# Optimization experiments

Measured on AMD Instinct MI355X. Metric: run time of the kernel, lower is better.

The kernel has to match this reference:

```python
import jax, jax.numpy as jnp
import numpy as np

R = 5   # num edge types
T = 3   # num node types
N = 50000
IN, HID, OUT = 256, 256, 128


def setup_inputs() -> dict:
    key = jax.random.key(0)
    ks = jax.random.split(key, 20)
    n0, n1, n2 = 16667, 16667, 16666
    x0 = jax.random.normal(ks[0], (n0, IN), jnp.float32)
    x1 = jax.random.normal(ks[1], (n1, IN), jnp.float32)
    emb2 = jax.random.normal(ks[2], (n2, IN), jnp.float32)  # learned embedding (xavier-like)
    E = 1600000
    edge_index = jax.random.randint(ks[3], (2, E), 0, N, dtype=jnp.int64)
    edge_type = jax.random.randint(ks[4], (E,), 0, R, dtype=jnp.int64)
    node_type = jax.random.randint(ks[5], (N,), 0, T, dtype=jnp.int64)
    local_node_idx = jax.random.randint(ks[6], (N,), 0, n2, dtype=jnp.int64)  # valid for all types

    def lin_w(k, o, i):
        return jax.random.normal(k, (o, i), jnp.float32) / np.sqrt(i).astype(np.float32)

    dims = [(IN, HID), (HID, HID), (HID, OUT)]
    params = {}
    ki = 7
    for l, (di, do) in enumerate(dims):
        params[f"rel_W{l}"] = jnp.stack([lin_w(jax.random.fold_in(ks[ki], r), do, di) for r in range(R)])
        params[f"root_W{l}"] = jnp.stack([lin_w(jax.random.fold_in(ks[ki + 1], t), do, di) for t in range(T)])
        params[f"root_b{l}"] = jnp.zeros((T, do), jnp.float32)
        ki += 2
    return dict(x0=x0, x1=x1, emb2=emb2,
                edge_index=edge_index, edge_type=edge_type,
                node_type=node_type, local_node_idx=local_node_idx, **params)


def _group_input(x_list, node_type, local_node_idx):
    # scatter per-type features into flat [N, IN]
    h = jnp.zeros((node_type.shape[0], x_list[0].shape[1]), x_list[0].dtype)
    for t, xt in enumerate(x_list):
        mask = (node_type == t)[:, None].astype(xt.dtype)
        h = h + mask * xt[local_node_idx]  # local_node_idx is always in-range
    return h


def _conv(x, rel_W, root_W, root_b, src, dst, edge_type, node_type):
    n = x.shape[0]
    # per-(target node, relation) mean aggregation in one segmented reduction
    seg = dst * R + edge_type
    msgs = x[src]                                              # [E, Din]
    sums = jax.ops.segment_sum(msgs, seg, num_segments=n * R)  # [N*R, Din]
    cnt = jax.ops.segment_sum(jnp.ones((seg.shape[0],), x.dtype), seg, num_segments=n * R)
    mean = (sums / jnp.maximum(cnt, 1.0)[:, None]).reshape(n, R, -1)
    out = jnp.einsum('nrd,rod->no', mean, rel_W)
    # per-node-type root transform (with bias)
    for t in range(T):
        mask = (node_type == t)[:, None].astype(x.dtype)
        out = out + mask * (x @ root_W[t].T + root_b[t])
    return out


def reference(x0, x1, emb2,
              rel_W0, root_W0, root_b0,
              rel_W1, root_W1, root_b1,
              rel_W2, root_W2, root_b2,
              edge_index, edge_type, node_type, local_node_idx):
    src, dst = edge_index[0], edge_index[1]
    x = _group_input([x0, x1, emb2], node_type, local_node_idx)
    layers = [(rel_W0, root_W0, root_b0), (rel_W1, root_W1, root_b1), (rel_W2, root_W2, root_b2)]
    for i, (rw, gw, gb) in enumerate(layers):
        x = _conv(x, rw, gw, gb, src, dst, edge_type, node_type)
        if i != len(layers) - 1:
            x = jax.nn.relu(x)  # eval mode: dropout is identity
    return jax.nn.log_softmax(x, axis=-1)
```

## Files before the change

### kernel.cpp

```cpp
#include <hip/hip_runtime.h>
#include <hip/hip_bf16.h>
#include <hip/hip_fp8.h>
#include <stdint.h>

#define N_NODES 50000
#define M_PAD   50048
#define N_EDGES 1600000
#define R_REL   5
#define NBUCK   391
#define NB1     256
#define EPB     6250
#define BH_N    (NBUCK * NB1)
#define GS_BLOCKS 98
#define STAGE_CAP 6144
#define HIST_BLOCKS 196

typedef __bf16 bf16;
typedef __bf16 bf16x2 __attribute__((ext_vector_type(2)));
typedef __bf16 bf16x4 __attribute__((ext_vector_type(4)));
typedef __bf16 bf16x8 __attribute__((ext_vector_type(8)));
typedef float  f32x2  __attribute__((ext_vector_type(2)));
typedef float  f32x4  __attribute__((ext_vector_type(4)));

#define GLOAD_LDS16(g, l)                                                          \
    __builtin_amdgcn_global_load_lds(                                              \
        (const __attribute__((address_space(1))) void*)(g),                        \
        (__attribute__((address_space(3))) void*)(l), 16, 0, 0)

__device__ __forceinline__ uint8_t f32_to_fp8(float f) {
    return __hip_fp8_e4m3(f).__x;
}
__device__ __forceinline__ float fp8_to_f32(uint32_t b) {
    __hip_fp8_e4m3 v; v.__x = (uint8_t)b; return (float)v;
}

__device__ __forceinline__ void fp8_accum4(uint32_t bits, float ww, float* s) {
#if __has_builtin(__builtin_amdgcn_cvt_pk_f32_fp8)
    f32x2 lo = __builtin_amdgcn_cvt_pk_f32_fp8((int)bits, false);
    f32x2 hi = __builtin_amdgcn_cvt_pk_f32_fp8((int)bits, true);
    s[0] += ww * lo[0]; s[1] += ww * lo[1];
    s[2] += ww * hi[0]; s[3] += ww * hi[1];
#else
    s[0] += ww * fp8_to_f32(bits & 0xFF);
    s[1] += ww * fp8_to_f32((bits >> 8) & 0xFF);
    s[2] += ww * fp8_to_f32((bits >> 16) & 0xFF);
    s[3] += ww * fp8_to_f32(bits >> 24);
#endif
}

__global__ __launch_bounds__(256) void group_input_k(
    const float* __restrict__ x0, const float* __restrict__ x1,
    const float* __restrict__ emb2, const int* __restrict__ ntype,
    const int* __restrict__ lidx, bf16* __restrict__ h)
{
    int row = blockIdx.x * 4 + (threadIdx.x >> 6);
    int lane = threadIdx.x & 63;
    if (row >= N_NODES) return;
    int t = ntype[row];
    int li = lidx[row];
    const float* src = (t == 0) ? x0 : (t == 1) ? x1 : emb2;
    float4 v = *reinterpret_cast<const float4*>(&src[(size_t)li * 256 + lane * 4]);
    bf16x4 o;
    o[0] = (bf16)v.x; o[1] = (bf16)v.y; o[2] = (bf16)v.z; o[3] = (bf16)v.w;
    *reinterpret_cast<bf16x4*>(&h[(size_t)row * 256 + lane * 4]) = o;
}

__global__ __launch_bounds__(256) void bucket_hist_k(
    const int* __restrict__ ei, int* __restrict__ bh)
{
    __shared__ int lds[NBUCK];
    int t = threadIdx.x;
    for (int i = t; i < NBUCK; i += 256) lds[i] = 0;
    __syncthreads();
    int base = blockIdx.x * EPB;
    for (int i = t; i < EPB; i += 256) {
        int dst = ei[N_EDGES + base + i];
        atomicAdd(&lds[dst >> 7], 1);
    }
    __syncthreads();
    for (int i = t; i < NBUCK; i += 256) bh[i * NB1 + blockIdx.x] = lds[i];
}

__global__ __launch_bounds__(256) void gscan1_k(
    const int* __restrict__ in, int* __restrict__ outv,
    int* __restrict__ blksum, int n)
{
    __shared__ int lds[256];
    int base = blockIdx.x * 1024;
    int t = threadIdx.x;
    int vals[4]; int s = 0;
#pragma unroll
    for (int i = 0; i < 4; ++i) {
        int idx = base + t * 4 + i;
        vals[i] = (idx < n) ? in[idx] : 0;
        s += vals[i];
    }
    lds[t] = s;
    __syncthreads();
    for (int off = 1; off < 256; off <<= 1) {
        int v = (t >= off) ? lds[t - off] : 0;
        __syncthreads();
        lds[t] += v;
        __syncthreads();
    }
    int incl = lds[t];
    int ex = incl - s;
    if (t == 255) blksum[blockIdx.x] = incl;
    int run = ex;
#pragma unroll
    for (int i = 0; i < 4; ++i) {
        int idx = base + t * 4 + i;
        if (idx < n) outv[idx] = run;
        run += vals[i];
    }
}

__global__ __launch_bounds__(256) void gscan2_k(int* __restrict__ blksum, int nblk)
{
    __shared__ int lds[256];
    int t = threadIdx.x;
    int v = (t < nblk) ? blksum[t] : 0;
    lds[t] = v;
    __syncthreads();
    for (int off = 1; off < 256; off <<= 1) {
        int u = (t >= off) ? lds[t - off] : 0;
        __syncthreads();
        lds[t] += u;
        __syncthreads();
    }
    if (t < nblk) blksum[t] = lds[t] - v;
}

__global__ __launch_bounds__(256) void gfold_k(
    int* __restrict__ outv, const int* __restrict__ blksum, int n)
{
    int base = blockIdx.x * 1024 + threadIdx.x * 4;
    int b = blksum[blockIdx.x];
#pragma unroll
    for (int i = 0; i < 4; ++i) {
        int idx = base + i;
        if (idx < n) outv[idx] += b;
    }
}

__global__ __launch_bounds__(256) void bucket_scatter_k(
    const int* __restrict__ ei, const int* __restrict__ et,
    const int* __restrict__ bhs, uint32_t* __restrict__ ebuf)
{
    __shared__ int cur[NBUCK];
    int t = threadIdx.x;
    for (int i = t; i < NBUCK; i += 256) cur[i] = bhs[i * NB1 + blockIdx.x];
    __syncthreads();
    int base = blockIdx.x * EPB;
    for (int i = t; i < EPB; i += 256) {
        int e = base + i;
        int src = ei[e];
        int dst = ei[N_EDGES + e];
        int r = et[e];
        int pos = atomicAdd(&cur[dst >> 7], 1);
        ebuf[pos] = (uint32_t)(src * R_REL + r) | ((uint32_t)(dst & 127) << 25);
    }
}

__global__ __launch_bounds__(256) void bucket_rank_k(
    const uint32_t* __restrict__ ebuf, const int* __restrict__ bhs,
    uint32_t* __restrict__ pk, int* __restrict__ noff)
{
    __shared__ uint32_t se[STAGE_CAP];
    __shared__ int hist[640];
    __shared__ int cursor[640];
    __shared__ int sb[256];
    int t = threadIdx.x;
    int b = blockIdx.x;
    int start = bhs[b * NB1];
    int end = (b < NBUCK - 1) ? bhs[(b + 1) * NB1] : N_EDGES;
    int size = end - start;
    for (int i = t; i < 640; i += 256) hist[i] = 0;
    __syncthreads();
    for (int i = t; i < size; i += 256) {
        uint32_t v = ebuf[start + i];
        if (i < STAGE_CAP) se[i] = v;
        uint32_t sr = v & 0x3FFFFu;
        int r = (int)(sr % 5u);
        int seg = (int)(v >> 25) * R_REL + r;
        atomicAdd(&hist[seg], 1);
    }
    __syncthreads();
    int b0 = t * 3;
    int loc[3]; int s0 = 0;
#pragma unroll
    for (int j = 0; j < 3; ++j) {
        int idx = b0 + j;
        int v = (idx < 640) ? hist[idx] : 0;
        loc[j] = s0; s0 += v;
    }
    sb[t] = s0;
    __syncthreads();
    for (int off = 1; off < 256; off <<= 1) {
        int u = (t >= off) ? sb[t - off] : 0;
        __syncthreads();
        sb[t] += u;
        __syncthreads();
    }
    int pre = sb[t] - s0;
#pragma unroll
    for (int j = 0; j < 3; ++j) {
        int idx = b0 + j;
        if (idx < 640) cursor[idx] = start + pre + loc[j];
    }
    __syncthreads();
    if (t < 128) noff[b * 128 + t] = cursor[t * 5];
    if (b == NBUCK - 1 && t == 128) noff[M_PAD] = N_EDGES;
    __syncthreads();
    for (int i = t; i < size; i += 256) {
        uint32_t v = (i < STAGE_CAP) ? se[i] : ebuf[start + i];
        uint32_t sr = v & 0x3FFFFu;
        int r = (int)(sr % 5u);
        int seg = (int)(v >> 25) * R_REL + r;
        int pos = atomicAdd(&cursor[seg], 1);
        pk[pos] = sr | ((uint32_t)hist[seg] << 18);
    }
}

__global__ __launch_bounds__(256) void typed_hist_k(
    const int* __restrict__ ntype, int* __restrict__ tcnt)
{
    __shared__ int c[3];
    if (threadIdx.x < 3) c[threadIdx.x] = 0;
    __syncthreads();
    int n = blockIdx.x * 256 + threadIdx.x;
    if (n < N_NODES) atomicAdd(&c[ntype[n]], 1);
    __syncthreads();
    if (threadIdx.x < 3) tcnt[threadIdx.x * HIST_BLOCKS + blockIdx.x] = c[threadIdx.x];
}

__global__ __launch_bounds__(1024) void typed_scan_k(
    const int* __restrict__ tcnt, int* __restrict__ toff, int* __restrict__ meta)
{
    __shared__ int lds[1024];
    int t = threadIdx.x;
    int v = (t < 3 * HIST_BLOCKS) ? tcnt[t] : 0;
    lds[t] = v;
    __syncthreads();
    for (int off = 1; off < 1024; off <<= 1) {
        int u = (t >= off) ? lds[t - off] : 0;
        __syncthreads();
        lds[t] += u;
        __syncthreads();
    }
    if (t < 3 * HIST_BLOCKS) toff[t] = lds[t] - v;
    if (t == 0) {
        int ts1 = lds[1 * HIST_BLOCKS - 1];
        int ts2 = lds[2 * HIST_BLOCKS - 1];
        int ts3 = lds[3 * HIST_BLOCKS - 1];
        meta[0] = 0; meta[1] = ts1; meta[2] = ts2; meta[3] = ts3;
        int c0 = ts1, c1 = ts2 - ts1, c2 = ts3 - ts2;
        meta[8] = c0; meta[9] = c1; meta[10] = c2;
        int b0 = (c0 + 127) >> 7, b1 = (c1 + 127) >> 7, b2 = (c2 + 127) >> 7;
        meta[4] = 0; meta[5] = b0; meta[6] = b0 + b1; meta[7] = b0 + b1 + b2;
    }
}

__global__ __launch_bounds__(256) void typed_scatter_k(
    const int* __restrict__ ntype, const int* __restrict__ toff,
    int* __restrict__ perm)
{
    __shared__ int cur[3];
    if (threadIdx.x < 3) cur[threadIdx.x] = 0;
    __syncthreads();
    int n = blockIdx.x * 256 + threadIdx.x;
    if (n < N_NODES) {
        int t = ntype[n];
        int rank = atomicAdd(&cur[t], 1);
        perm[toff[t * HIST_BLOCKS + blockIdx.x] + rank] = n;
    }
}

__global__ __launch_bounds__(256) void cast_w_k(
    const float* __restrict__ relW, const float* __restrict__ rootW,
    bf16* __restrict__ Wt, bf16* __restrict__ Rt, int relN, int rootN)
{
    int i = blockIdx.x * 256 + threadIdx.x;
    if (i < relN)  Wt[i] = (bf16)relW[i];
    if (i < rootN) Rt[i] = (bf16)rootW[i];
}

__global__ __launch_bounds__(256) void gemm_y_f8_k(
    const bf16* __restrict__ A, const bf16* __restrict__ B,
    uint8_t* __restrict__ Y, int ldc, int NT)
{
    __shared__ bf16 As[128][64];
    __shared__ bf16 Bs[128][64];
    int bid = blockIdx.x;
    int xcd = bid & 7;
    int r2 = bid >> 3;
    int ml = r2 / NT, nt = r2 - ml * NT;
    int m = xcd * 49 + ml;
    if (m >= M_PAD / 128) return;
    int m0 = m * 128, n0 = nt * 128;
    int tid = threadIdx.x;
    int lane = tid & 63, wave = tid >> 6;
    int wm = wave >> 1, wn = wave & 1;

    f32x4 acc[4][4] = {};

    for (int kt = 0; kt < 4; ++kt) {
#pragma unroll
        for (int cc = 0; cc < 4; ++cc) {
            int linear = cc * 256 + tid;
            int row = linear >> 3, sl = linear & 7;
            const bf16* gA = &A[(size_t)(m0 + row) * 256 + kt * 64 + sl * 8];
            const bf16* gB = &B[(size_t)(n0 + row) * 256 + kt * 64 + sl * 8];
            char* sA = (char*)&As[0][0] + (size_t)(cc * 256 + wave * 64) * 16;
            char* sB = (char*)&Bs[0][0] + (size_t)(cc * 256 + wave * 64) * 16;
            GLOAD_LDS16(gA, sA);
            GLOAD_LDS16(gB, sB);
        }
        __syncthreads();
#pragma unroll
        for (int kk = 0; kk < 2; ++kk) {
            bf16x8 af[4], bfr[4];
            int k0 = kk * 32 + (lane >> 4) * 8;
#pragma unroll
            for (int i = 0; i < 4; ++i) {
                af[i]  = *reinterpret_cast<const bf16x8*>(&As[wm * 64 + i * 16 + (lane & 15)][k0]);
                bfr[i] = *reinterpret_cast<const bf16x8*>(&Bs[wn * 64 + i * 16 + (lane & 15)][k0]);
            }
#pragma unroll
            for (int i = 0; i < 4; ++i)
#pragma unroll
                for (int j = 0; j < 4; ++j)
                    acc[i][j] = __builtin_amdgcn_mfma_f32_16x16x32_bf16(af[i], bfr[j], acc[i][j], 0, 0, 0);
        }
        __syncthreads();
    }

#pragma unroll
    for (int i = 0; i < 4; ++i)
#pragma unroll
        for (int j = 0; j < 4; ++j)
#pragma unroll
            for (int r = 0; r < 4; ++r) {
                int row = m0 + wm * 64 + i * 16 + (lane >> 4) * 4 + r;
                int col = n0 + wn * 64 + j * 16 + (lane & 15);
                Y[(size_t)row * ldc + col] = f32_to_fp8(acc[i][j][r]);
            }
}

__global__ __launch_bounds__(256) void gemm_y_bf_k(
    const bf16* __restrict__ A, const bf16* __restrict__ B,
    bf16* __restrict__ Y, int ldc, int NT)
{
    __shared__ bf16 As[128][64];
    __shared__ bf16 Bs[128][64];
    int bid = blockIdx.x;
    int xcd = bid & 7;
    int r2 = bid >> 3;
    int ml = r2 / NT, nt = r2 - ml * NT;
    int m = xcd * 49 + ml;
    if (m >= M_PAD / 128) return;
    int m0 = m * 128, n0 = nt * 128;
    int tid = threadIdx.x;
    int lane = tid & 63, wave = tid >> 6;
    int wm = wave >> 1, wn = wave & 1;

    f32x4 acc[4][4] = {};

    for (int kt = 0; kt < 4; ++kt) {
#pragma unroll
        for (int cc = 0; cc < 4; ++cc) {
            int linear = cc * 256 + tid;
            int row = linear >> 3, sl = linear & 7;
            const bf16* gA = &A[(size_t)(m0 + row) * 256 + kt * 64 + sl * 8];
            const bf16* gB = &B[(size_t)(n0 + row) * 256 + kt * 64 + sl * 8];
            char* sA = (char*)&As[0][0] + (size_t)(cc * 256 + wave * 64) * 16;
            char* sB = (char*)&Bs[0][0] + (size_t)(cc * 256 + wave * 64) * 16;
            GLOAD_LDS16(gA, sA);
            GLOAD_LDS16(gB, sB);
        }
        __syncthreads();
#pragma unroll
        for (int kk = 0; kk < 2; ++kk) {
            bf16x8 af[4], bfr[4];
            int k0 = kk * 32 + (lane >> 4) * 8;
#pragma unroll
            for (int i = 0; i < 4; ++i) {
                af[i]  = *reinterpret_cast<const bf16x8*>(&As[wm * 64 + i * 16 + (lane & 15)][k0]);
                bfr[i] = *reinterpret_cast<const bf16x8*>(&Bs[wn * 64 + i * 16 + (lane & 15)][k0]);
            }
#pragma unroll
            for (int i = 0; i < 4; ++i)
#pragma unroll
                for (int j = 0; j < 4; ++j)
                    acc[i][j] = __builtin_amdgcn_mfma_f32_16x16x32_bf16(af[i], bfr[j], acc[i][j], 0, 0, 0);
        }
        __syncthreads();
    }

#pragma unroll
    for (int i = 0; i < 4; ++i)
#pragma unroll
        for (int j = 0; j < 4; ++j)
#pragma unroll
            for (int r = 0; r < 4; ++r) {
                int row = m0 + wm * 64 + i * 16 + (lane >> 4) * 4 + r;
                int col = n0 + wn * 64 + j * 16 + (lane & 15);
                Y[(size_t)row * ldc + col] = (bf16)acc[i][j][r];
            }
}

__global__ __launch_bounds__(256) void gather_f8_k(
    const uint8_t* __restrict__ Y, const uint32_t* __restrict__ pk,
    const int* __restrict__ noff, bf16* __restrict__ Cb)
{
    int wave = threadIdx.x >> 6, lane = threadIdx.x & 63;
    int n = blockIdx.x * 4 + wave;
    if (n >= N_NODES) return;
    int off0 = noff[n];
    int c = noff[n + 1] - off0;

    float s[4] = {};
    int e = 0;
    for (; e + 16 <= c; e += 16) {
        uint32_t w[16]; uint32_t v[16];
#pragma unroll
        for (int j = 0; j < 16; ++j) w[j] = pk[off0 + e + j];
#pragma unroll
        for (int j = 0; j < 16; ++j)
            v[j] = *reinterpret_cast<const uint32_t*>(&Y[(size_t)(w[j] & 0x3FFFF) * 256 + lane * 4]);
#pragma unroll
        for (int j = 0; j < 16; ++j) {
            float ww = __builtin_amdgcn_rcpf((float)(w[j] >> 18));
            fp8_accum4(v[j], ww, s);
        }
    }
    if (e + 8 <= c) {
        uint32_t w[8]; uint32_t v[8];
#pragma unroll
        for (int j = 0; j < 8; ++j) w[j] = pk[off0 + e + j];
#pragma unroll
        for (int j = 0; j < 8; ++j)
            v[j] = *reinterpret_cast<const uint32_t*>(&Y[(size_t)(w[j] & 0x3FFFF) * 256 + lane * 4]);
#pragma unroll
        for (int j = 0; j < 8; ++j) {
            float ww = __builtin_amdgcn_rcpf((float)(w[j] >> 18));
            fp8_accum4(v[j], ww, s);
        }
        e += 8;
    }
    if (e + 4 <= c) {
        uint32_t w[4]; uint32_t v[4];
#pragma unroll
        for (int j = 0; j < 4; ++j) w[j] = pk[off0 + e + j];
#pragma unroll
        for (int j = 0; j < 4; ++j)
            v[j] = *reinterpret_cast<const uint32_t*>(&Y[(size_t)(w[j] & 0x3FFFF) * 256 + lane * 4]);
#pragma unroll
        for (int j = 0; j < 4; ++j) {
            float ww = __builtin_amdgcn_rcpf((float)(w[j] >> 18));
            fp8_accum4(v[j], ww, s);
        }
        e += 4;
    }
    for (; e < c; ++e) {
        uint32_t w = pk[off0 + e];
        uint32_t v = *reinterpret_cast<const uint32_t*>(&Y[(size_t)(w & 0x3FFFF) * 256 + lane * 4]);
        float ww = __builtin_amdgcn_rcpf((float)(w >> 18));
        fp8_accum4(v, ww, s);
    }

    bf16x4 o;
#pragma unroll
    for (int q = 0; q < 4; ++q) o[q] = (bf16)s[q];
    *reinterpret_cast<bf16x4*>(&Cb[(size_t)n * 256 + lane * 4]) = o;
}

__global__ __launch_bounds__(256) void gather_bf_k(
    const bf16* __restrict__ Y, const uint32_t* __restrict__ pk,
    const int* __restrict__ noff, bf16* __restrict__ Cb)
{
    int wave = threadIdx.x >> 6, lane = threadIdx.x & 63;
    int n = blockIdx.x * 4 + wave;
    if (n >= N_NODES) return;
    int off0 = noff[n];
    int c = noff[n + 1] - off0;

    float s0 = 0.f, s1 = 0.f;
    int e = 0;
    for (; e + 16 <= c; e += 16) {
        uint32_t w[16]; bf16x2 v[16];
#pragma unroll
        for (int j = 0; j < 16; ++j) w[j] = pk[off0 + e + j];
#pragma unroll
        for (int j = 0; j < 16; ++j)
            v[j] = *reinterpret_cast<const bf16x2*>(&Y[(size_t)(w[j] & 0x3FFFF) * 128 + lane * 2]);
#pragma unroll
        for (int j = 0; j < 16; ++j) {
            float ww = __builtin_amdgcn_rcpf((float)(w[j] >> 18));
            s0 += ww * (float)v[j][0];
            s1 += ww * (float)v[j][1];
        }
    }
    if (e + 8 <= c) {
        uint32_t w[8]; bf16x2 v[8];
#pragma unroll
        for (int j = 0; j < 8; ++j) w[j] = pk[off0 + e + j];
#pragma unroll
        for (int j = 0; j < 8; ++j)
            v[j] = *reinterpret_cast<const bf16x2*>(&Y[(size_t)(w[j] & 0x3FFFF) * 128 + lane * 2]);
#pragma unroll
        for (int j = 0; j < 8; ++j) {
            float ww = __builtin_amdgcn_rcpf((float)(w[j] >> 18));
            s0 += ww * (float)v[j][0];
            s1 += ww * (float)v[j][1];
        }
        e += 8;
    }
    if (e + 4 <= c) {
        uint32_t w[4]; bf16x2 v[4];
#pragma unroll
        for (int j = 0; j < 4; ++j) w[j] = pk[off0 + e + j];
#pragma unroll
        for (int j = 0; j < 4; ++j)
            v[j] = *reinterpret_cast<const bf16x2*>(&Y[(size_t)(w[j] & 0x3FFFF) * 128 + lane * 2]);
#pragma unroll
        for (int j = 0; j < 4; ++j) {
            float ww = __builtin_amdgcn_rcpf((float)(w[j] >> 18));
            s0 += ww * (float)v[j][0];
            s1 += ww * (float)v[j][1];
        }
        e += 4;
    }
    for (; e < c; ++e) {
        uint32_t w = pk[off0 + e];
        bf16x2 v = *reinterpret_cast<const bf16x2*>(&Y[(size_t)(w & 0x3FFFF) * 128 + lane * 2]);
        float ww = __builtin_amdgcn_rcpf((float)(w >> 18));
        s0 += ww * (float)v[0];
        s1 += ww * (float)v[1];
    }

    bf16x2 o; o[0] = (bf16)s0; o[1] = (bf16)s1;
    *reinterpret_cast<bf16x2*>(&Cb[(size_t)n * 128 + lane * 2]) = o;
}

__global__ __launch_bounds__(256) void gemm_root_k(
    const bf16* __restrict__ h, const bf16* __restrict__ Rt,
    const float* __restrict__ rootB, const int* __restrict__ perm,
    const int* __restrict__ meta, const bf16* __restrict__ Cb,
    float* __restrict__ C, bf16* __restrict__ hout, int Dout, int relu_mode)
{
    __shared__ bf16 As[128][64];
    __shared__ bf16 Bs[128][64];
    __shared__ int ridx[128];
    int tid = threadIdx.x;
    int bx = blockIdx.x;
    int b1 = meta[5], b2 = meta[6], b3 = meta[7];
    if (bx >= b3) return;
    int t = (bx >= b2) ? 2 : (bx >= b1 ? 1 : 0);
    int chunk = bx - (t == 2 ? b2 : (t == 1 ? b1 : 0));
    int tstart = meta[t];
    int tc = meta[8 + t];
    int rbase = chunk * 128;
    if (tid < 128) {
        int lr = rbase + tid;
        ridx[tid] = (lr < tc) ? perm[tstart + lr] : 0;
    }
    __syncthreads();

    int lane = tid & 63, wave = tid >> 6;
    int wm = wave >> 1, wn = wave & 1;
    int n0 = blockIdx.y * 128;
    const bf16* B = Rt + (size_t)t * Dout * 256;

    f32x4 acc[4][4] = {};

    for (int kt = 0; kt < 4; ++kt) {
#pragma unroll
        for (int cc = 0; cc < 4; ++cc) {
            int linear = cc * 256 + tid;
            int row = linear >> 3, sl = linear & 7;
            const bf16* gA = &h[(size_t)ridx[row] * 256 + kt * 64 + sl * 8];
            const bf16* gB = &B[(size_t)(n0 + row) * 256 + kt * 64 + sl * 8];
            char* sA = (char*)&As[0][0] + (size_t)(cc * 256 + wave * 64) * 16;
            char* sB = (char*)&Bs[0][0] + (size_t)(cc * 256 + wave * 64) * 16;
            GLOAD_LDS16(gA, sA);
            GLOAD_LDS16(gB, sB);
        }
        __syncthreads();
#pragma unroll
        for (int kk = 0; kk < 2; ++kk) {
            bf16x8 af[4], bfr[4];
            int k0 = kk * 32 + (lane >> 4) * 8;
#pragma unroll
            for (int i = 0; i < 4; ++i) {
                af[i]  = *reinterpret_cast<const bf16x8*>(&As[wm * 64 + i * 16 + (lane & 15)][k0]);
                bfr[i] = *reinterpret_cast<const bf16x8*>(&Bs[wn * 64 + i * 16 + (lane & 15)][k0]);
            }
#pragma unroll
            for (int i = 0; i < 4; ++i)
#pragma unroll
                for (int j = 0; j < 4; ++j)
                    acc[i][j] = __builtin_amdgcn_mfma_f32_16x16x32_bf16(af[i], bfr[j], acc[i][j], 0, 0, 0);
        }
        __syncthreads();
    }

#pragma unroll
    for (int i = 0; i < 4; ++i)
#pragma unroll
        for (int j = 0; j < 4; ++j)
#pragma unroll
            for (int r = 0; r < 4; ++r) {
                int rl = wm * 64 + i * 16 + (lane >> 4) * 4 + r;
                int col = n0 + wn * 64 + j * 16 + (lane & 15);
                if (rbase + rl < tc) {
                    int ri = ridx[rl];
                    float v = (float)Cb[(size_t)ri * Dout + col] + acc[i][j][r]
                              + rootB[t * Dout + col];
                    if (relu_mode)
                        hout[(size_t)ri * Dout + col] = (bf16)fmaxf(v, 0.f);
                    else
                        C[(size_t)ri * Dout + col] = v;
                }
            }
}

__global__ __launch_bounds__(256) void logsoftmax_k(
    const float* __restrict__ C, float* __restrict__ out, int M)
{
    int row = blockIdx.x * 4 + (threadIdx.x >> 6);
    int lane = threadIdx.x & 63;
    if (row >= M) return;
    float v0 = C[(size_t)row * 128 + lane];
    float v1 = C[(size_t)row * 128 + 64 + lane];
    float m = fmaxf(v0, v1);
    for (int off = 32; off; off >>= 1) m = fmaxf(m, __shfl_xor(m, off));
    float s = expf(v0 - m) + expf(v1 - m);
    for (int off = 32; off; off >>= 1) s += __shfl_xor(s, off);
    float lse = m + logf(s);
    out[(size_t)row * 128 + lane] = v0 - lse;
    out[(size_t)row * 128 + 64 + lane] = v1 - lse;
}

extern "C" void kernel_launch(void* const* d_in, const int* in_sizes, int n_in,
                              void* d_out, int out_size, void* d_ws, size_t ws_size,
                              hipStream_t stream)
{
    const float* x0   = (const float*)d_in[0];
    const float* x1   = (const float*)d_in[1];
    const float* emb2 = (const float*)d_in[2];
    const int*   ei   = (const int*)d_in[3];
    const int*   et   = (const int*)d_in[4];
    const int*   ntyp = (const int*)d_in[5];
    const int*   lidx = (const int*)d_in[6];
    const float* relW[3]  = {(const float*)d_in[7],  (const float*)d_in[10], (const float*)d_in[13]};
    const float* rootW[3] = {(const float*)d_in[8],  (const float*)d_in[11], (const float*)d_in[14]};
    const float* rootB[3] = {(const float*)d_in[9],  (const float*)d_in[12], (const float*)d_in[15]};
    float* out = (float*)d_out;

    char* p = (char*)d_ws;
    auto carve = [&](size_t bytes) {
        char* q = p;
        p += (bytes + 255) & ~(size_t)255;
        return (void*)q;
    };
    bf16* h_a   = (bf16*)carve((size_t)M_PAD * 256 * 2);
    bf16* h_b   = (bf16*)carve((size_t)M_PAD * 256 * 2);
    uint8_t* Yq = (uint8_t*)carve((size_t)M_PAD * 1280);
    bf16* Yb    = (bf16*)Yq;
    bf16* Cb    = (bf16*)carve((size_t)M_PAD * 256 * 2);
    float* C    = (float*)carve((size_t)M_PAD * 128 * 4);
    bf16* WtA   = (bf16*)carve((size_t)(2 * R_REL * 256 * 256 + R_REL * 128 * 256) * 2);
    bf16* RtA   = (bf16*)carve((size_t)(2 * 3 * 256 * 256 + 3 * 128 * 256) * 2);
    int* bh     = (int*)carve((size_t)BH_N * 4);
    int* bhs    = (int*)carve((size_t)BH_N * 4);
    int* gblk   = (int*)carve((size_t)256 * 4);
    uint32_t* ebuf = (uint32_t*)carve((size_t)N_EDGES * 4);
    uint32_t* pk   = (uint32_t*)carve((size_t)N_EDGES * 4);
    int* noff   = (int*)carve((size_t)(M_PAD + 1) * 4);
    int* tcnt   = (int*)carve((size_t)3 * HIST_BLOCKS * 4);
    int* toff   = (int*)carve((size_t)3 * HIST_BLOCKS * 4);
    int* meta   = (int*)carve((size_t)16 * 4);
    int* perm   = (int*)carve((size_t)N_NODES * 4);

    bf16* Wt[3] = {WtA, WtA + (size_t)R_REL * 256 * 256, WtA + (size_t)2 * R_REL * 256 * 256};
    bf16* Rt[3] = {RtA, RtA + (size_t)3 * 256 * 256, RtA + (size_t)2 * 3 * 256 * 256};

    group_input_k<<<(N_NODES + 3) / 4, 256, 0, stream>>>(x0, x1, emb2, ntyp, lidx, h_a);
    bucket_hist_k<<<NB1, 256, 0, stream>>>(ei, bh);
    gscan1_k<<<GS_BLOCKS, 256, 0, stream>>>(bh, bhs, gblk, BH_N);
    gscan2_k<<<1, 256, 0, stream>>>(gblk, GS_BLOCKS);
    gfold_k<<<GS_BLOCKS, 256, 0, stream>>>(bhs, gblk, BH_N);
    bucket_scatter_k<<<NB1, 256, 0, stream>>>(ei, et, bhs, ebuf);
    bucket_rank_k<<<NBUCK, 256, 0, stream>>>(ebuf, bhs, pk, noff);
    typed_hist_k<<<HIST_BLOCKS, 256, 0, stream>>>(ntyp, tcnt);
    typed_scan_k<<<1, 1024, 0, stream>>>(tcnt, toff, meta);
    typed_scatter_k<<<HIST_BLOCKS, 256, 0, stream>>>(ntyp, toff, perm);
    const int douts[3] = {256, 256, 128};
    for (int l = 0; l < 3; ++l)
        cast_w_k<<<(R_REL * douts[l] * 256 + 255) / 256, 256, 0, stream>>>(
            relW[l], rootW[l], Wt[l], Rt[l], R_REL * douts[l] * 256, 3 * douts[l] * 256);

    bf16* cur = h_a;
    bf16* nxt = h_b;
    for (int l = 0; l < 3; ++l) {
        if (l < 2) {
            gemm_y_f8_k<<<49 * 10 * 8, 256, 0, stream>>>(cur, Wt[l], Yq, 1280, 10);
            gather_f8_k<<<(N_NODES + 3) / 4, 256, 0, stream>>>(Yq, pk, noff, Cb);
            gemm_root_k<<<dim3(393, 2), 256, 0, stream>>>(
                cur, Rt[l], rootB[l], perm, meta, Cb, C, nxt, 256, 1);
        } else {
            gemm_y_bf_k<<<49 * 5 * 8, 256, 0, stream>>>(cur, Wt[l], Yb, 640, 5);
            gather_bf_k<<<(N_NODES + 3) / 4, 256, 0, stream>>>(Yb, pk, noff, Cb);
            gemm_root_k<<<dim3(393, 1), 256, 0, stream>>>(
                cur, Rt[l], rootB[l], perm, meta, Cb, C, nxt, 128, 0);
        }
        bf16* tmp = cur; cur = nxt; nxt = tmp;
    }
    logsoftmax_k<<<(N_NODES + 3) / 4, 256, 0, stream>>>(C, out, N_NODES);
}
```

Baseline: 525.5 us.

## Merge setup kernels, fuse log-softmax into final root GEMM, pack fp8 conversions

Merges the independent preprocessing kernels (input grouping, bucket histogram, type histogram, weight casts) into one block-indexed launch. It also combines the two small scans and the fold/typed scatter steps, cutting the number of kernel launches. Log-softmax is fused into the last root GEMM through an LDS tile, so the fp32 intermediate no longer makes a round trip to global memory. FP8 output quantization now uses packed conversion instructions. The costs are higher LDS use in the final GEMM (64KB for the L tile), which lowers occupancy, and an in-place scan on bh.

```diff
diff --git a/kernel.cpp b/kernel.cpp
--- a/kernel.cpp
+++ b/kernel.cpp
@@ -14,6 +14,7 @@
 #define GS_BLOCKS 98
 #define STAGE_CAP 6144
 #define HIST_BLOCKS 196
+#define GI_BLOCKS 12500
 
 typedef __bf16 bf16;
 typedef __bf16 bf16x2 __attribute__((ext_vector_type(2)));
@@ -32,6 +33,17 @@
 }
 __device__ __forceinline__ float fp8_to_f32(uint32_t b) {
     __hip_fp8_e4m3 v; v.__x = (uint8_t)b; return (float)v;
+}
+
+__device__ __forceinline__ uint32_t fp8_pack4(float a0, float a1, float a2, float a3) {
+#if __has_builtin(__builtin_amdgcn_cvt_pk_fp8_f32)
+    int q = __builtin_amdgcn_cvt_pk_fp8_f32(a0, a1, 0, false);
+    q = __builtin_amdgcn_cvt_pk_fp8_f32(a2, a3, q, true);
+    return (uint32_t)q;
+#else
+    return (uint32_t)f32_to_fp8(a0) | ((uint32_t)f32_to_fp8(a1) << 8) |
+           ((uint32_t)f32_to_fp8(a2) << 16) | ((uint32_t)f32_to_fp8(a3) << 24);
+#endif
 }
 
 __device__ __forceinline__ void fp8_accum4(uint32_t bits, float ww, float* s) {
@@ -48,37 +60,67 @@
 #endif
 }
 
-__global__ __launch_bounds__(256) void group_input_k(
+__global__ __launch_bounds__(256) void setup1_k(
     const float* __restrict__ x0, const float* __restrict__ x1,
     const float* __restrict__ emb2, const int* __restrict__ ntype,
-    const int* __restrict__ lidx, bf16* __restrict__ h)
-{
-    int row = blockIdx.x * 4 + (threadIdx.x >> 6);
-    int lane = threadIdx.x & 63;
-    if (row >= N_NODES) return;
-    int t = ntype[row];
-    int li = lidx[row];
-    const float* src = (t == 0) ? x0 : (t == 1) ? x1 : emb2;
-    float4 v = *reinterpret_cast<const float4*>(&src[(size_t)li * 256 + lane * 4]);
-    bf16x4 o;
-    o[0] = (bf16)v.x; o[1] = (bf16)v.y; o[2] = (bf16)v.z; o[3] = (bf16)v.w;
-    *reinterpret_cast<bf16x4*>(&h[(size_t)row * 256 + lane * 4]) = o;
-}
-
-__global__ __launch_bounds__(256) void bucket_hist_k(
-    const int* __restrict__ ei, int* __restrict__ bh)
-{
-    __shared__ int lds[NBUCK];
+    const int* __restrict__ lidx, bf16* __restrict__ h,
+    const int* __restrict__ ei, int* __restrict__ bh,
+    int* __restrict__ tcnt,
+    const float* __restrict__ relW0, const float* __restrict__ rootW0,
+    const float* __restrict__ relW1, const float* __restrict__ rootW1,
+    const float* __restrict__ relW2, const float* __restrict__ rootW2,
+    bf16* __restrict__ Wt0, bf16* __restrict__ Rt0,
+    bf16* __restrict__ Wt1, bf16* __restrict__ Rt1,
+    bf16* __restrict__ Wt2, bf16* __restrict__ Rt2)
+{
+    __shared__ int smem[NBUCK];
+    int bid = blockIdx.x;
     int t = threadIdx.x;
-    for (int i = t; i < NBUCK; i += 256) lds[i] = 0;
-    __syncthreads();
-    int base = blockIdx.x * EPB;
-    for (int i = t; i < EPB; i += 256) {
-        int dst = ei[N_EDGES + base + i];
-        atomicAdd(&lds[dst >> 7], 1);
-    }
-    __syncthreads();
-    for (int i = t; i < NBUCK; i += 256) bh[i * NB1 + blockIdx.x] = lds[i];
+    if (bid < GI_BLOCKS) {
+        int row = bid * 4 + (t >> 6);
+        int lane = t & 63;
+        int ty = ntype[row];
+        int li = lidx[row];
+        const float* src = (ty == 0) ? x0 : (ty == 1) ? x1 : emb2;
+        float4 v = *reinterpret_cast<const float4*>(&src[(size_t)li * 256 + lane * 4]);
+        bf16x4 o;
+        o[0] = (bf16)v.x; o[1] = (bf16)v.y; o[2] = (bf16)v.z; o[3] = (bf16)v.w;
+        *reinterpret_cast<bf16x4*>(&h[(size_t)row * 256 + lane * 4]) = o;
+        return;
+    }
+    bid -= GI_BLOCKS;
+    if (bid < NB1) {
+        for (int i = t; i < NBUCK; i += 256) smem[i] = 0;
+        __syncthreads();
+        int base = bid * EPB;
+        for (int i = t; i < EPB; i += 256) {
+            int dst = ei[N_EDGES + base + i];
+            atomicAdd(&smem[dst >> 7], 1);
+        }
+        __syncthreads();
+        for (int i = t; i < NBUCK; i += 256) bh[i * NB1 + bid] = smem[i];
+        return;
+    }
+    bid -= NB1;
+    if (bid < HIST_BLOCKS) {
+        if (t < 3) smem[t] = 0;
+        __syncthreads();
+        int n = bid * 256 + t;
+        if (n < N_NODES) atomicAdd(&smem[ntype[n]], 1);
+        __syncthreads();
+        if (t < 3) tcnt[t * HIST_BLOCKS + bid] = smem[t];
+        return;
+    }
+    bid -= HIST_BLOCKS;
+    const float* relW; const float* rootW; bf16* Wt; bf16* Rt; int Dout;
+    if (bid < 1280)      { relW = relW0; rootW = rootW0; Wt = Wt0; Rt = Rt0; Dout = 256; }
+    else if (bid < 2560) { relW = relW1; rootW = rootW1; Wt = Wt1; Rt = Rt1; Dout = 256; bid -= 1280; }
+    else                 { relW = relW2; rootW = rootW2; Wt = Wt2; Rt = Rt2; Dout = 128; bid -= 2560; }
+    int i = bid * 256 + t;
+    int relN = R_REL * Dout * 256;
+    if (i < relN)  Wt[i] = (bf16)relW[i];
+    int rootN = 3 * Dout * 256;
+    if (i < rootN) Rt[i] = (bf16)rootW[i];
 }
 
 __global__ __launch_bounds__(256) void gscan1_k(
@@ -115,31 +157,73 @@
     }
 }
 
-__global__ __launch_bounds__(256) void gscan2_k(int* __restrict__ blksum, int nblk)
-{
-    __shared__ int lds[256];
+__global__ __launch_bounds__(1024) void scan2m_k(
+    int* __restrict__ gblk,
+    const int* __restrict__ tcnt, int* __restrict__ toff, int* __restrict__ meta)
+{
+    __shared__ int lds[1024];
     int t = threadIdx.x;
-    int v = (t < nblk) ? blksum[t] : 0;
+    if (blockIdx.x == 0) {
+        int v = (t < GS_BLOCKS) ? gblk[t] : 0;
+        lds[t] = v;
+        __syncthreads();
+        for (int off = 1; off < 1024; off <<= 1) {
+            int u = (t >= off) ? lds[t - off] : 0;
+            __syncthreads();
+            lds[t] += u;
+            __syncthreads();
+        }
+        if (t < GS_BLOCKS) gblk[t] = lds[t] - v;
+        return;
+    }
+    int v = (t < 3 * HIST_BLOCKS) ? tcnt[t] : 0;
     lds[t] = v;
     __syncthreads();
-    for (int off = 1; off < 256; off <<= 1) {
+    for (int off = 1; off < 1024; off <<= 1) {
         int u = (t >= off) ? lds[t - off] : 0;
         __syncthreads();
         lds[t] += u;
         __syncthreads();
     }
-    if (t < nblk) blksum[t] = lds[t] - v;
-}
-
-__global__ __launch_bounds__(256) void gfold_k(
-    int* __restrict__ outv, const int* __restrict__ blksum, int n)
-{
-    int base = blockIdx.x * 1024 + threadIdx.x * 4;
-    int b = blksum[blockIdx.x];
-#pragma unroll
-    for (int i = 0; i < 4; ++i) {
-        int idx = base + i;
-        if (idx < n) outv[idx] += b;
+    if (t < 3 * HIST_BLOCKS) toff[t] = lds[t] - v;
+    if (t == 0) {
+        int ts1 = lds[1 * HIST_BLOCKS - 1];
+        int ts2 = lds[2 * HIST_BLOCKS - 1];
+        int ts3 = lds[3 * HIST_BLOCKS - 1];
+        meta[0] = 0; meta[1] = ts1; meta[2] = ts2; meta[3] = ts3;
+        int c0 = ts1, c1 = ts2 - ts1, c2 = ts3 - ts2;
+        meta[8] = c0; meta[9] = c1; meta[10] = c2;
+        int b0 = (c0 + 127) >> 7, b1 = (c1 + 127) >> 7, b2 = (c2 + 127) >> 7;
+        meta[4] = 0; meta[5] = b0; meta[6] = b0 + b1; meta[7] = b0 + b1 + b2;
+    }
+}
+
+__global__ __launch_bounds__(256) void setup3_k(
+    int* __restrict__ bhs, const int* __restrict__ gblk,
+    const int* __restrict__ ntype, const int* __restrict__ toff,
+    int* __restrict__ perm)
+{
+    __shared__ int cur[3];
+    int bid = blockIdx.x;
+    int t = threadIdx.x;
+    if (bid < GS_BLOCKS) {
+        int base = bid * 1024 + t * 4;
+        int b = gblk[bid];
+#pragma unroll
+        for (int i = 0; i < 4; ++i) {
+            int idx = base + i;
+            if (idx < BH_N) bhs[idx] += b;
+        }
+        return;
+    }
+    bid -= GS_BLOCKS;
+    if (t < 3) cur[t] = 0;
+    __syncthreads();
+    int n = bid * 256 + t;
+    if (n < N_NODES) {
+        int ty = ntype[n];
+        int rank = atomicAdd(&cur[ty], 1);
+        perm[toff[ty * HIST_BLOCKS + bid] + rank] = n;
     }
 }
 
@@ -220,69 +304,6 @@
         int pos = atomicAdd(&cursor[seg], 1);
         pk[pos] = sr | ((uint32_t)hist[seg] << 18);
     }
-}
-
-__global__ __launch_bounds__(256) void typed_hist_k(
-    const int* __restrict__ ntype, int* __restrict__ tcnt)
-{
-    __shared__ int c[3];
-    if (threadIdx.x < 3) c[threadIdx.x] = 0;
-    __syncthreads();
-    int n = blockIdx.x * 256 + threadIdx.x;
-    if (n < N_NODES) atomicAdd(&c[ntype[n]], 1);
-    __syncthreads();
-    if (threadIdx.x < 3) tcnt[threadIdx.x * HIST_BLOCKS + blockIdx.x] = c[threadIdx.x];
-}
-
-__global__ __launch_bounds__(1024) void typed_scan_k(
-    const int* __restrict__ tcnt, int* __restrict__ toff, int* __restrict__ meta)
-{
-    __shared__ int lds[1024];
-    int t = threadIdx.x;
-    int v = (t < 3 * HIST_BLOCKS) ? tcnt[t] : 0;
-    lds[t] = v;
-    __syncthreads();
-    for (int off = 1; off < 1024; off <<= 1) {
-        int u = (t >= off) ? lds[t - off] : 0;
-        __syncthreads();
-        lds[t] += u;
-        __syncthreads();
-    }
-    if (t < 3 * HIST_BLOCKS) toff[t] = lds[t] - v;
-    if (t == 0) {
-        int ts1 = lds[1 * HIST_BLOCKS - 1];
-        int ts2 = lds[2 * HIST_BLOCKS - 1];
-        int ts3 = lds[3 * HIST_BLOCKS - 1];
-        meta[0] = 0; meta[1] = ts1; meta[2] = ts2; meta[3] = ts3;
-        int c0 = ts1, c1 = ts2 - ts1, c2 = ts3 - ts2;
-        meta[8] = c0; meta[9] = c1; meta[10] = c2;
-        int b0 = (c0 + 127) >> 7, b1 = (c1 + 127) >> 7, b2 = (c2 + 127) >> 7;
-        meta[4] = 0; meta[5] = b0; meta[6] = b0 + b1; meta[7] = b0 + b1 + b2;
-    }
-}
-
-__global__ __launch_bounds__(256) void typed_scatter_k(
-    const int* __restrict__ ntype, const int* __restrict__ toff,
-    int* __restrict__ perm)
-{
-    __shared__ int cur[3];
-    if (threadIdx.x < 3) cur[threadIdx.x] = 0;
-    __syncthreads();
-    int n = blockIdx.x * 256 + threadIdx.x;
-    if (n < N_NODES) {
-        int t = ntype[n];
-        int rank = atomicAdd(&cur[t], 1);
-        perm[toff[t * HIST_BLOCKS + blockIdx.x] + rank] = n;
-    }
-}
-
-__global__ __launch_bounds__(256) void cast_w_k(
-    const float* __restrict__ relW, const float* __restrict__ rootW,
-    bf16* __restrict__ Wt, bf16* __restrict__ Rt, int relN, int rootN)
-{
-    int i = blockIdx.x * 256 + threadIdx.x;
-    if (i < relN)  Wt[i] = (bf16)relW[i];
-    if (i < rootN) Rt[i] = (bf16)rootW[i];
 }
 
 __global__ __launch_bounds__(256) void gemm_y_f8_k(
@@ -338,13 +359,15 @@
 #pragma unroll
     for (int i = 0; i < 4; ++i)
 #pragma unroll
-        for (int j = 0; j < 4; ++j)
-#pragma unroll
-            for (int r = 0; r < 4; ++r) {
-                int row = m0 + wm * 64 + i * 16 + (lane >> 4) * 4 + r;
-                int col = n0 + wn * 64 + j * 16 + (lane & 15);
-                Y[(size_t)row * ldc + col] = f32_to_fp8(acc[i][j][r]);
-            }
+        for (int j = 0; j < 4; ++j) {
+            uint32_t q = fp8_pack4(acc[i][j][0], acc[i][j][1], acc[i][j][2], acc[i][j][3]);
+            int row0 = m0 + wm * 64 + i * 16 + (lane >> 4) * 4;
+            int col = n0 + wn * 64 + j * 16 + (lane & 15);
+            Y[(size_t)(row0 + 0) * ldc + col] = (uint8_t)q;
+            Y[(size_t)(row0 + 1) * ldc + col] = (uint8_t)(q >> 8);
+            Y[(size_t)(row0 + 2) * ldc + col] = (uint8_t)(q >> 16);
+            Y[(size_t)(row0 + 3) * ldc + col] = (uint8_t)(q >> 24);
+        }
 }
 
 __global__ __launch_bounds__(256) void gemm_y_bf_k(
@@ -547,7 +570,7 @@
     const bf16* __restrict__ h, const bf16* __restrict__ Rt,
     const float* __restrict__ rootB, const int* __restrict__ perm,
     const int* __restrict__ meta, const bf16* __restrict__ Cb,
-    float* __restrict__ C, bf16* __restrict__ hout, int Dout, int relu_mode)
+    bf16* __restrict__ hout, int Dout)
 {
     __shared__ bf16 As[128][64];
     __shared__ bf16 Bs[128][64];
@@ -617,29 +640,102 @@
                     int ri = ridx[rl];
                     float v = (float)Cb[(size_t)ri * Dout + col] + acc[i][j][r]
                               + rootB[t * Dout + col];
-                    if (relu_mode)
-                        hout[(size_t)ri * Dout + col] = (bf16)fmaxf(v, 0.f);
-                    else
-                        C[(size_t)ri * Dout + col] = v;
+                    hout[(size_t)ri * Dout + col] = (bf16)fmaxf(v, 0.f);
                 }
             }
 }
 
-__global__ __launch_bounds__(256) void logsoftmax_k(
-    const float* __restrict__ C, float* __restrict__ out, int M)
-{
-    int row = blockIdx.x * 4 + (threadIdx.x >> 6);
-    int lane = threadIdx.x & 63;
-    if (row >= M) return;
-    float v0 = C[(size_t)row * 128 + lane];
-    float v1 = C[(size_t)row * 128 + 64 + lane];
-    float m = fmaxf(v0, v1);
-    for (int off = 32; off; off >>= 1) m = fmaxf(m, __shfl_xor(m, off));
-    float s = expf(v0 - m) + expf(v1 - m);
-    for (int off = 32; off; off >>= 1) s += __shfl_xor(s, off);
-    float lse = m + logf(s);
-    out[(size_t)row * 128 + lane] = v0 - lse;
-    out[(size_t)row * 128 + 64 + lane] = v1 - lse;
+__global__ __launch_bounds__(256) void gemm_root_ls_k(
+    const bf16* __restrict__ h, const bf16* __restrict__ Rt,
+    const float* __restrict__ rootB, const int* __restrict__ perm,
+    const int* __restrict__ meta, const bf16* __restrict__ Cb,
+    float* __restrict__ out)
+{
+    __shared__ bf16 As[128][64];
+    __shared__ bf16 Bs[128][64];
+    __shared__ int ridx[128];
+    __shared__ float L[128][128];
+    const int Dout = 128;
+    int tid = threadIdx.x;
+    int bx = blockIdx.x;
+    int b1 = meta[5], b2 = meta[6], b3 = meta[7];
+    if (bx >= b3) return;
+    int t = (bx >= b2) ? 2 : (bx >= b1 ? 1 : 0);
+    int chunk = bx - (t == 2 ? b2 : (t == 1 ? b1 : 0));
+    int tstart = meta[t];
+    int tc = meta[8 + t];
+    int rbase = chunk * 128;
+    if (tid < 128) {
+        int lr = rbase + tid;
+        ridx[tid] = (lr < tc) ? perm[tstart + lr] : 0;
+    }
+    __syncthreads();
+
+    int lane = tid & 63, wave = tid >> 6;
+    int wm = wave >> 1, wn = wave & 1;
+    const bf16* B = Rt + (size_t)t * Dout * 256;
+
+    f32x4 acc[4][4] = {};
+
+    for (int kt = 0; kt < 4; ++kt) {
+#pragma unroll
+        for (int cc = 0; cc < 4; ++cc) {
+            int linear = cc * 256 + tid;
+            int row = linear >> 3, sl = linear & 7;
+            const bf16* gA = &h[(size_t)ridx[row] * 256 + kt * 64 + sl * 8];
+            const bf16* gB = &B[(size_t)(row) * 256 + kt * 64 + sl * 8];
+            char* sA = (char*)&As[0][0] + (size_t)(cc * 256 + wave * 64) * 16;
+            char* sB = (char*)&Bs[0][0] + (size_t)(cc * 256 + wave * 64) * 16;
+            GLOAD_LDS16(gA, sA);
+            GLOAD_LDS16(gB, sB);
+        }
+        __syncthreads();
+#pragma unroll
+        for (int kk = 0; kk < 2; ++kk) {
+            bf16x8 af[4], bfr[4];
+            int k0 = kk * 32 + (lane >> 4) * 8;
+#pragma unroll
+            for (int i = 0; i < 4; ++i) {
+                af[i]  = *reinterpret_cast<const bf16x8*>(&As[wm * 64 + i * 16 + (lane & 15)][k0]);
+                bfr[i] = *reinterpret_cast<const bf16x8*>(&Bs[wn * 64 + i * 16 + (lane & 15)][k0]);
+            }
+#pragma unroll
+            for (int i = 0; i < 4; ++i)
+#pragma unroll
+                for (int j = 0; j < 4; ++j)
+                    acc[i][j] = __builtin_amdgcn_mfma_f32_16x16x32_bf16(af[i], bfr[j], acc[i][j], 0, 0, 0);
+        }
+        __syncthreads();
+    }
+
+#pragma unroll
+    for (int i = 0; i < 4; ++i)
+#pragma unroll
+        for (int j = 0; j < 4; ++j)
+#pragma unroll
+            for (int r = 0; r < 4; ++r) {
+                int rl = wm * 64 + i * 16 + (lane >> 4) * 4 + r;
+                int col = wn * 64 + j * 16 + (lane & 15);
+                int ri = ridx[rl];
+                L[rl][col] = (float)Cb[(size_t)ri * Dout + col] + acc[i][j][r]
+                             + rootB[t * Dout + col];
+            }
+    __syncthreads();
+
+    for (int rr = 0; rr < 32; ++rr) {
+        int row = wave * 32 + rr;
+        if (rbase + row >= tc) continue;
+        float v0 = L[row][lane];
+        float v1 = L[row][64 + lane];
+        float m = fmaxf(v0, v1);
+        for (int off = 32; off; off >>= 1) m = fmaxf(m, __shfl_xor(m, off));
+        float s = expf(v0 - m) + expf(v1 - m);
+        for (int off = 32; off; off >>= 1) s += __shfl_xor(s, off);
+        float lse = m + logf(s);
+        int ri = ridx[row];
+        out[(size_t)ri * 128 + lane] = v0 - lse;
+        out[(size_t)ri * 128 + 64 + lane] = v1 - lse;
+    }
 }
 
 extern "C" void kernel_launch(void* const* d_in, const int* in_sizes, int n_in,
@@ -669,11 +765,9 @@
     uint8_t* Yq = (uint8_t*)carve((size_t)M_PAD * 1280);
     bf16* Yb    = (bf16*)Yq;
     bf16* Cb    = (bf16*)carve((size_t)M_PAD * 256 * 2);
-    float* C    = (float*)carve((size_t)M_PAD * 128 * 4);
     bf16* WtA   = (bf16*)carve((size_t)(2 * R_REL * 256 * 256 + R_REL * 128 * 256) * 2);
     bf16* RtA   = (bf16*)carve((size_t)(2 * 3 * 256 * 256 + 3 * 128 * 256) * 2);
     int* bh     = (int*)carve((size_t)BH_N * 4);
-    int* bhs    = (int*)carve((size_t)BH_N * 4);
     int* gblk   = (int*)carve((size_t)256 * 4);
     uint32_t* ebuf = (uint32_t*)carve((size_t)N_EDGES * 4);
     uint32_t* pk   = (uint32_t*)carve((size_t)N_EDGES * 4);
@@ -686,36 +780,26 @@
     bf16* Wt[3] = {WtA, WtA + (size_t)R_REL * 256 * 256, WtA + (size_t)2 * R_REL * 256 * 256};
     bf16* Rt[3] = {RtA, RtA + (size_t)3 * 256 * 256, RtA + (size_t)2 * 3 * 256 * 256};
 
-    group_input_k<<<(N_NODES + 3) / 4, 256, 0, stream>>>(x0, x1, emb2, ntyp, lidx, h_a);
-    bucket_hist_k<<<NB1, 256, 0, stream>>>(ei, bh);
-    gscan1_k<<<GS_BLOCKS, 256, 0, stream>>>(bh, bhs, gblk, BH_N);
-    gscan2_k<<<1, 256, 0, stream>>>(gblk, GS_BLOCKS);
-    gfold_k<<<GS_BLOCKS, 256, 0, stream>>>(bhs, gblk, BH_N);
-    bucket_scatter_k<<<NB1, 256, 0, stream>>>(ei, et, bhs, ebuf);
-    bucket_rank_k<<<NBUCK, 256, 0, stream>>>(ebuf, bhs, pk, noff);
-    typed_hist_k<<<HIST_BLOCKS, 256, 0, stream>>>(ntyp, tcnt);
-    typed_scan_k<<<1, 1024, 0, stream>>>(tcnt, toff, meta);
-    typed_scatter_k<<<HIST_BLOCKS, 256, 0, stream>>>(ntyp, toff, perm);
-    const int douts[3] = {256, 256, 128};
-    for (int l = 0; l < 3; ++l)
-        cast_w_k<<<(R_REL * douts[l] * 256 + 255) / 256, 256, 0, stream>>>(
-            relW[l], rootW[l], Wt[l], Rt[l], R_REL * douts[l] * 256, 3 * douts[l] * 256);
+    setup1_k<<<GI_BLOCKS + NB1 + HIST_BLOCKS + 3200, 256, 0, stream>>>(
+        x0, x1, emb2, ntyp, lidx, h_a, ei, bh, tcnt,
+        relW[0], rootW[0], relW[1], rootW[1], relW[2], rootW[2],
+        Wt[0], Rt[0], Wt[1], Rt[1], Wt[2], Rt[2]);
+    gscan1_k<<<GS_BLOCKS, 256, 0, stream>>>(bh, bh, gblk, BH_N);
+    scan2m_k<<<2, 1024, 0, stream>>>(gblk, tcnt, toff, meta);
+    setup3_k<<<GS_BLOCKS + HIST_BLOCKS, 256, 0, stream>>>(bh, gblk, ntyp, toff, perm);
+    bucket_scatter_k<<<NB1, 256, 0, stream>>>(ei, et, bh, ebuf);
+    bucket_rank_k<<<NBUCK, 256, 0, stream>>>(ebuf, bh, pk, noff);
 
     bf16* cur = h_a;
     bf16* nxt = h_b;
-    for (int l = 0; l < 3; ++l) {
-        if (l < 2) {
-            gemm_y_f8_k<<<49 * 10 * 8, 256, 0, stream>>>(cur, Wt[l], Yq, 1280, 10);
-            gather_f8_k<<<(N_NODES + 3) / 4, 256, 0, stream>>>(Yq, pk, noff, Cb);
-            gemm_root_k<<<dim3(393, 2), 256, 0, stream>>>(
-                cur, Rt[l], rootB[l], perm, meta, Cb, C, nxt, 256, 1);
-        } else {
-            gemm_y_bf_k<<<49 * 5 * 8, 256, 0, stream>>>(cur, Wt[l], Yb, 640, 5);
-            gather_bf_k<<<(N_NODES + 3) / 4, 256, 0, stream>>>(Yb, pk, noff, Cb);
-            gemm_root_k<<<dim3(393, 1), 256, 0, stream>>>(
-                cur, Rt[l], rootB[l], perm, meta, Cb, C, nxt, 128, 0);
-        }
+    for (int l = 0; l < 2; ++l) {
+        gemm_y_f8_k<<<49 * 10 * 8, 256, 0, stream>>>(cur, Wt[l], Yq, 1280, 10);
+        gather_f8_k<<<GI_BLOCKS, 256, 0, stream>>>(Yq, pk, noff, Cb);
+        gemm_root_k<<<dim3(393, 2), 256, 0, stream>>>(
+            cur, Rt[l], rootB[l], perm, meta, Cb, nxt, 256);
         bf16* tmp = cur; cur = nxt; nxt = tmp;
     }
-    logsoftmax_k<<<(N_NODES + 3) / 4, 256, 0, stream>>>(C, out, N_NODES);
-}
+    gemm_y_bf_k<<<49 * 5 * 8, 256, 0, stream>>>(cur, Wt[2], Yb, 640, 5);
+    gather_bf_k<<<GI_BLOCKS, 256, 0, stream>>>(Yb, pk, noff, Cb);
+    gemm_root_ls_k<<<393, 256, 0, stream>>>(cur, Rt[2], rootB[2], perm, meta, Cb, out);
+}
```

Measured after the change: 520.9 us. Within noise of the previous version (-0.9%).
